# Kernel tuning notes

Hardware: AMD Instinct MI355X
Metric: run time of the kernel (lower is better)

The kernel has to match this reference:

```python
import jax, jax.numpy as jnp
import numpy as np

N_NODES = 100000
N_EDGES = 1600000
IN_C, HID_C, OUT_C = 256, 128, 256


def setup_inputs() -> dict:
    key = jax.random.key(0)
    ks = jax.random.split(key, 8)
    x = jax.random.normal(ks[0], (N_NODES, IN_C), dtype=jnp.float32)
    src = jax.random.randint(ks[1], (N_EDGES,), 0, N_NODES, dtype=jnp.int64)
    dst = jnp.sort(jax.random.randint(ks[2], (N_EDGES,), 0, N_NODES, dtype=jnp.int64))
    # GraphConv weight [in, hid] (glorot), bias [hid]
    W_conv = jax.random.normal(ks[3], (IN_C, HID_C), dtype=jnp.float32) * (2.0 / (IN_C + HID_C)) ** 0.5
    b_conv = jnp.zeros((HID_C,), dtype=jnp.float32)
    # torch Linear weights are [out, in]
    W1 = jax.random.normal(ks[4], (HID_C, HID_C), dtype=jnp.float32) * (2.0 / (2 * HID_C)) ** 0.5
    b1 = jax.random.uniform(ks[5], (HID_C,), dtype=jnp.float32, minval=-1.0, maxval=1.0) / np.sqrt(HID_C)
    W2 = jax.random.normal(ks[6], (OUT_C, HID_C), dtype=jnp.float32) * (2.0 / (HID_C + OUT_C)) ** 0.5
    b2 = jax.random.uniform(ks[7], (OUT_C,), dtype=jnp.float32, minval=-1.0, maxval=1.0) / np.sqrt(OUT_C)
    return {"x": x, "src": src, "dst": dst, "W_conv": W_conv, "b_conv": b_conv,
            "W1": W1, "b1": b1, "W2": W2, "b2": b2}


def reference(x, src, dst, W_conv, b_conv, W1, b1, W2, b2):
    N = x.shape[0]
    ones = jnp.ones(src.shape[0], dtype=x.dtype)
    out_deg = jnp.clip(jax.ops.segment_sum(ones, src, num_segments=N), 1.0)  # [N]
    in_deg = jnp.clip(jax.ops.segment_sum(ones, dst, num_segments=N), 1.0)   # [N]
    # DGL GraphConv, norm='both', in_feats > out_feats -> weight applied before aggregation
    h = x * jax.lax.rsqrt(out_deg)[:, None]          # src-side normalization
    h = h @ W_conv                                    # [N, hid]
    m = jax.ops.segment_sum(h[src], dst, num_segments=N, indices_are_sorted=True)
    h = m * jax.lax.rsqrt(in_deg)[:, None] + b_conv   # dst-side normalization + bias
    h = jax.nn.relu(h)
    h = jax.nn.relu(h @ W1.T + b1)
    return h @ W2.T + b2
```

## Files before the change

### kernel.cpp

```cpp
#include <hip/hip_runtime.h>
#include <hip/hip_bf16.h>


typedef __attribute__((ext_vector_type(8))) short short8;
typedef __attribute__((ext_vector_type(4))) float f32x4;

static __device__ __forceinline__ float bf2f(unsigned int u16) {
    union { unsigned int i; float f; } c; c.i = u16 << 16; return c.f;
}
static __device__ __forceinline__ ushort f2bf(float f) {
    union { float f; unsigned int i; } c; c.f = f;
    unsigned int i = c.i;
    return (ushort)((i + 0x7FFFu + ((i >> 16) & 1u)) >> 16);
}

constexpr int NCHUNK   = 256;
constexpr int NBUK_MAX = 512;
constexpr int WPREP_BLOCKS = (128 * 256 + 128 * 128 + 256 * 128) / 256;

__global__ __launch_bounds__(256) void prep_kernel(
    const float* __restrict__ Wc, const float* __restrict__ W1,
    const float* __restrict__ W2, ushort* __restrict__ WcT,
    ushort* __restrict__ W1b, ushort* __restrict__ W2b,
    const int* __restrict__ src, int* __restrict__ M,
    const int* __restrict__ dst, int* __restrict__ row_ptr,
    int nE, int N, int nBuk, int chunkSz)
{
    __shared__ int cnt[NBUK_MAX];
    const int bid = blockIdx.x, tid = threadIdx.x;

    if (bid < WPREP_BLOCKS) {
        int i = bid * 256 + tid;
        if (i < 128 * 256) {
            int o = i >> 8, k = i & 255;
            WcT[o * 256 + k] = f2bf(Wc[k * 128 + o]);
        } else if (i < 128 * 256 + 128 * 128) {
            int j = i - 128 * 256;
            W1b[j] = f2bf(W1[j]);
        } else {
            int j = i - 128 * 256 - 128 * 128;
            W2b[j] = f2bf(W2[j]);
        }
        return;
    }
    if (bid < WPREP_BLOCKS + NCHUNK) {
        int c = bid - WPREP_BLOCKS;
        for (int i = tid; i < nBuk; i += 256) cnt[i] = 0;
        __syncthreads();
        int e0 = c * chunkSz, e1 = min(e0 + chunkSz, nE);
        for (int e = e0 + tid; e < e1; e += 256)
            atomicAdd(&cnt[src[e] >> 8], 1);
        __syncthreads();
        for (int b = tid; b < nBuk; b += 256)
            M[b * NCHUNK + c] = cnt[b];
        return;
    }
    int e = (bid - WPREP_BLOCKS - NCHUNK) * 256 + tid;
    if (e >= nE) return;
    int d = dst[e];
    if (e == 0) {
        for (int n = 0; n <= d; ++n) row_ptr[n] = 0;
    } else {
        int p = dst[e - 1];
        for (int n = p + 1; n <= d; ++n) row_ptr[n] = e;
    }
    if (e == nE - 1) {
        for (int n = d + 1; n <= N; ++n) row_ptr[n] = nE;
    }
}

__global__ __launch_bounds__(256) void scanA_kernel(
    int* __restrict__ M, int* __restrict__ tot)
{
    __shared__ int buf[2][NCHUNK];
    int b = blockIdx.x, tid = threadIdx.x;
    int v = M[b * NCHUNK + tid];
    buf[0][tid] = v;
    __syncthreads();
    int pi = 0;
#pragma unroll
    for (int off = 1; off < NCHUNK; off <<= 1) {
        int t = buf[pi][tid];
        if (tid >= off) t += buf[pi][tid - off];
        buf[pi ^ 1][tid] = t;
        __syncthreads();
        pi ^= 1;
    }
    int incl = buf[pi][tid];
    M[b * NCHUNK + tid] = incl - v;
    if (tid == NCHUNK - 1) tot[b] = incl;
}

static __device__ __forceinline__ void scan_bb(
    const int* __restrict__ tot, int* bb_l, int nBuk, int tid)
{
    if (tid < 64) {
        int base = 0;
        for (int i0 = 0; i0 < nBuk; i0 += 64) {
            int i = i0 + tid;
            int v = (i < nBuk) ? tot[i] : 0;
            int orig = v;
#pragma unroll
            for (int off = 1; off < 64; off <<= 1) {
                int u = __shfl_up(v, off, 64);
                if (tid >= off) v += u;
            }
            if (i < nBuk) bb_l[i] = base + v - orig;
            base += __shfl(v, 63, 64);
        }
        if (tid == 0) bb_l[nBuk] = base;
    }
    __syncthreads();
}

__global__ __launch_bounds__(256) void scatter_keys_kernel(
    const int* __restrict__ src, const int* __restrict__ M,
    const int* __restrict__ tot, int* __restrict__ ss,
    int nE, int nBuk, int chunkSz)
{
    __shared__ int cur[NBUK_MAX];
    __shared__ int bb_l[NBUK_MAX + 1];
    int c = blockIdx.x, tid = threadIdx.x;
    scan_bb(tot, bb_l, nBuk, tid);
    for (int i = tid; i < nBuk; i += 256)
        cur[i] = M[i * NCHUNK + c] + bb_l[i];
    __syncthreads();
    int e0 = c * chunkSz, e1 = min(e0 + chunkSz, nE);
    for (int e = e0 + tid; e < e1; e += 256) {
        int s = src[e];
        int pos = atomicAdd(&cur[s >> 8], 1);
        ss[pos] = s;
    }
}

__global__ __launch_bounds__(512, 4) void gemm1_kernel(
    const float* __restrict__ A, const ushort* __restrict__ B,
    const int* __restrict__ ss, const int* __restrict__ tot,
    ushort* __restrict__ C, int nRows, int nBuk)
{
    __shared__ ushort Bs[128 * 256];
    __shared__ ushort As[128 * 32];
    __shared__ int hist[128];
    __shared__ int eRange[2];

    const int tid  = threadIdx.x;
    const int lane = tid & 63;
    const int w    = tid >> 6;
    const int wm   = w >> 1;
    const int wn   = w & 1;
    const int r    = lane & 15;
    const int q    = lane >> 4;
    const int row0 = blockIdx.x * 128;

#pragma unroll
    for (int s = 0; s < 8; ++s) {
        int idx = s * 512 + tid;
        int col = idx >> 5, kg = idx & 31;
        *(short8*)&Bs[col * 256 + ((kg ^ (col & 7)) * 8)] =
            *(const short8*)&B[(size_t)col * 256 + kg * 8];
    }
    if (tid < 128) hist[tid] = 0;

    if (w == 0) {
        int bk = blockIdx.x >> 1;
        int partial = 0;
        for (int i = lane; i < bk; i += 64) partial += tot[i];
#pragma unroll
        for (int off = 32; off >= 1; off >>= 1)
            partial += __shfl_xor(partial, off, 64);
        if (lane == 0) {
            eRange[0] = partial;
            eRange[1] = partial + tot[bk];
        }
    }

    const int arow = tid >> 2, akg = tid & 3;
    const int aslot = (akg ^ ((arow >> 1) & 3)) * 8;

    float4 areg[3][2];

#define G1_ISSUE(cc, bb)                                                     \
    {                                                                        \
        int g0 = row0 + arow;                                                \
        areg[bb][0] = make_float4(0.f, 0.f, 0.f, 0.f);                       \
        areg[bb][1] = make_float4(0.f, 0.f, 0.f, 0.f);                       \
        if (g0 < nRows) {                                                    \
            const float* p = &A[(size_t)g0 * 256 + (cc) * 32 + akg * 8];     \
            areg[bb][0] = *(const float4*)p;                                 \
            areg[bb][1] = *(const float4*)(p + 4);                           \
        }                                                                    \
    }

    G1_ISSUE(0, 0)
    G1_ISSUE(1, 1)
    G1_ISSUE(2, 2)
    __syncthreads();

    {
        int e0 = eRange[0], e1 = eRange[1];
        for (int e = e0 + tid; e < e1; e += 512) {
            int s = ss[e];
            if ((s >> 7) == blockIdx.x)
                atomicAdd(&hist[s & 127], 1);
        }
    }

    f32x4 acc[8];
#pragma unroll
    for (int t = 0; t < 8; ++t) acc[t] = (f32x4){0.f, 0.f, 0.f, 0.f};

#pragma unroll
    for (int c = 0; c < 8; ++c) {
        if (c > 0) __syncthreads();
        const int buf = c % 3;
        {
            float4 v0 = areg[buf][0], v1 = areg[buf][1];
            ushort u[8];
            u[0] = f2bf(v0.x); u[1] = f2bf(v0.y); u[2] = f2bf(v0.z); u[3] = f2bf(v0.w);
            u[4] = f2bf(v1.x); u[5] = f2bf(v1.y); u[6] = f2bf(v1.z); u[7] = f2bf(v1.w);
            *(short8*)&As[arow * 32 + aslot] = *(const short8*)u;
        }
        if (c + 3 < 8) G1_ISSUE(c + 3, buf)
        __syncthreads();
        {
            int ra0 = wm * 32 + r, ra1 = wm * 32 + 16 + r;
            short8 a0 = *(const short8*)&As[ra0 * 32 + ((q ^ ((ra0 >> 1) & 3)) * 8)];
            short8 a1 = *(const short8*)&As[ra1 * 32 + ((q ^ ((ra1 >> 1) & 3)) * 8)];
            int sB = c * 4 + q;
#pragma unroll
            for (int t = 0; t < 4; ++t) {
                int col = wn * 64 + t * 16 + r;
                short8 b = *(const short8*)&Bs[col * 256 + ((sB ^ (col & 7)) * 8)];
                acc[t]     = __builtin_amdgcn_mfma_f32_16x16x32_bf16(a0, b, acc[t], 0, 0, 0);
                acc[4 + t] = __builtin_amdgcn_mfma_f32_16x16x32_bf16(a1, b, acc[4 + t], 0, 0, 0);
            }
        }
    }
#undef G1_ISSUE

#pragma unroll
    for (int fr = 0; fr < 2; ++fr)
#pragma unroll
        for (int t = 0; t < 4; ++t) {
            int col = wn * 64 + t * 16 + r;
#pragma unroll
            for (int reg = 0; reg < 4; ++reg) {
                int lr = wm * 32 + fr * 16 + q * 4 + reg;
                int g = row0 + lr;
                if (g < nRows) {
                    float sc = rsqrtf((float)max(hist[lr], 1));
                    C[(size_t)g * 128 + col] = f2bf(acc[fr * 4 + t][reg] * sc);
                }
            }
        }
}

static __device__ __forceinline__ void acc8(float* a, uint4 u) {
    union { unsigned int i; float f; } c;
    c.i = u.x << 16;          a[0] += c.f;
    c.i = u.x & 0xffff0000u;  a[1] += c.f;
    c.i = u.y << 16;          a[2] += c.f;
    c.i = u.y & 0xffff0000u;  a[3] += c.f;
    c.i = u.z << 16;          a[4] += c.f;
    c.i = u.z & 0xffff0000u;  a[5] += c.f;
    c.i = u.w << 16;          a[6] += c.f;
    c.i = u.w & 0xffff0000u;  a[7] += c.f;
}

__global__ __launch_bounds__(256) void gather_kernel(
    const ushort* __restrict__ h1, const int* __restrict__ src,
    const int* __restrict__ rp, const float* __restrict__ b_conv,
    ushort* __restrict__ h2, int N)
{
    int n = (blockIdx.x * 256 + threadIdx.x) >> 6;
    int lane = threadIdx.x & 63;
    if (n >= N) return;
    const int g = lane >> 4;
    const int c = lane & 15;
    int e0 = rp[n], e1 = rp[n + 1];

    float a[8];
#pragma unroll
    for (int j = 0; j < 8; ++j) a[j] = 0.f;

    int e = e0 + g;
    for (; e + 12 < e1; e += 16) {
        int s0 = src[e], s1 = src[e + 4], s2 = src[e + 8], s3 = src[e + 12];
        uint4 u0 = *(const uint4*)&h1[((size_t)(unsigned)s0 << 7) + c * 8];
        uint4 u1 = *(const uint4*)&h1[((size_t)(unsigned)s1 << 7) + c * 8];
        uint4 u2 = *(const uint4*)&h1[((size_t)(unsigned)s2 << 7) + c * 8];
        uint4 u3 = *(const uint4*)&h1[((size_t)(unsigned)s3 << 7) + c * 8];
        acc8(a, u0); acc8(a, u1); acc8(a, u2); acc8(a, u3);
    }
    for (; e < e1; e += 4) {
        uint4 u0 = *(const uint4*)&h1[((size_t)(unsigned)src[e] << 7) + c * 8];
        acc8(a, u0);
    }

#pragma unroll
    for (int j = 0; j < 8; ++j) {
        a[j] += __shfl_xor(a[j], 16, 64);
        a[j] += __shfl_xor(a[j], 32, 64);
    }

    if (g == 0) {
        float sc = rsqrtf((float)max(e1 - e0, 1));
        ushort o[8];
#pragma unroll
        for (int j = 0; j < 8; ++j)
            o[j] = f2bf(fmaxf(fmaf(a[j], sc, b_conv[c * 8 + j]), 0.f));
        *(short8*)&h2[((size_t)(unsigned)n << 7) + c * 8] = *(const short8*)o;
    }
}

__global__ __launch_bounds__(512) void gemm23_kernel(
    const ushort* __restrict__ A, const ushort* __restrict__ W1b,
    const ushort* __restrict__ W2b, const float* __restrict__ b1,
    const float* __restrict__ b2, float* __restrict__ out, int nRows)
{
    __shared__ ushort AsTs[128 * 128];
    __shared__ ushort Ws[128 * 128];

    const int tid  = threadIdx.x;
    const int lane = tid & 63;
    const int w    = tid >> 6;
    const int wm   = w >> 1;
    const int wn   = w & 1;
    const int r    = lane & 15;
    const int q    = lane >> 4;
    const int row0 = blockIdx.x * 128;

#pragma unroll
    for (int s = 0; s < 4; ++s) {
        int idx = s * 512 + tid;
        int row = idx >> 4, kg = idx & 15;
        int g = row0 + row;
        short8 v = (short8){0, 0, 0, 0, 0, 0, 0, 0};
        if (g < nRows) v = *(const short8*)&A[(size_t)g * 128 + kg * 8];
        *(short8*)&AsTs[row * 128 + ((kg ^ (row & 7)) * 8)] = v;
    }
#pragma unroll
    for (int s = 0; s < 4; ++s) {
        int idx = s * 512 + tid;
        int col = idx >> 4, kg = idx & 15;
        *(short8*)&Ws[col * 128 + ((kg ^ (col & 7)) * 8)] =
            *(const short8*)&W1b[(size_t)col * 128 + kg * 8];
    }
    __syncthreads();

    f32x4 acc1[8];
#pragma unroll
    for (int t = 0; t < 8; ++t) acc1[t] = (f32x4){0.f, 0.f, 0.f, 0.f};
#pragma unroll
    for (int ks = 0; ks < 4; ++ks) {
        int sA = ks * 4 + q;
        int ra0 = wm * 32 + r, ra1 = wm * 32 + 16 + r;
        short8 a0 = *(const short8*)&AsTs[ra0 * 128 + ((sA ^ (ra0 & 7)) * 8)];
        short8 a1 = *(const short8*)&AsTs[ra1 * 128 + ((sA ^ (ra1 & 7)) * 8)];
#pragma unroll
        for (int t = 0; t < 4; ++t) {
            int col = wn * 64 + t * 16 + r;
            short8 b = *(const short8*)&Ws[col * 128 + ((sA ^ (col & 7)) * 8)];
            acc1[t]     = __builtin_amdgcn_mfma_f32_16x16x32_bf16(a0, b, acc1[t], 0, 0, 0);
            acc1[4 + t] = __builtin_amdgcn_mfma_f32_16x16x32_bf16(a1, b, acc1[4 + t], 0, 0, 0);
        }
    }
    __syncthreads();

#pragma unroll
    for (int fr = 0; fr < 2; ++fr)
#pragma unroll
        for (int t = 0; t < 4; ++t) {
            int col = wn * 64 + t * 16 + r;
            float bo = b1[col];
#pragma unroll
            for (int reg = 0; reg < 4; ++reg) {
                int row = wm * 32 + fr * 16 + q * 4 + reg;
                float v = fmaxf(acc1[fr * 4 + t][reg] + bo, 0.f);
                AsTs[row * 128 + (((col >> 3) ^ (row & 7)) * 8) + (col & 7)] = f2bf(v);
            }
        }
#pragma unroll
    for (int s = 0; s < 4; ++s) {
        int idx = s * 512 + tid;
        int col = idx >> 4, kg = idx & 15;
        *(short8*)&Ws[col * 128 + ((kg ^ (col & 7)) * 8)] =
            *(const short8*)&W2b[(size_t)col * 128 + kg * 8];
    }
    __syncthreads();

    f32x4 acc2[16];
#pragma unroll
    for (int t = 0; t < 16; ++t) acc2[t] = (f32x4){0.f, 0.f, 0.f, 0.f};
#pragma unroll
    for (int ks = 0; ks < 4; ++ks) {
        int sA = ks * 4 + q;
        int ra0 = wm * 32 + r, ra1 = wm * 32 + 16 + r;
        short8 a0 = *(const short8*)&AsTs[ra0 * 128 + ((sA ^ (ra0 & 7)) * 8)];
        short8 a1 = *(const short8*)&AsTs[ra1 * 128 + ((sA ^ (ra1 & 7)) * 8)];
#pragma unroll
        for (int t = 0; t < 4; ++t) {
            int col = wn * 64 + t * 16 + r;
            short8 b = *(const short8*)&Ws[col * 128 + ((sA ^ (col & 7)) * 8)];
            acc2[t]     = __builtin_amdgcn_mfma_f32_16x16x32_bf16(a0, b, acc2[t], 0, 0, 0);
            acc2[4 + t] = __builtin_amdgcn_mfma_f32_16x16x32_bf16(a1, b, acc2[4 + t], 0, 0, 0);
        }
    }
    __syncthreads();

#pragma unroll
    for (int s = 0; s < 4; ++s) {
        int idx = s * 512 + tid;
        int col = idx >> 4, kg = idx & 15;
        *(short8*)&Ws[col * 128 + ((kg ^ (col & 7)) * 8)] =
            *(const short8*)&W2b[(size_t)(128 + col) * 128 + kg * 8];
    }
    __syncthreads();

#pragma unroll
    for (int ks = 0; ks < 4; ++ks) {
        int sA = ks * 4 + q;
        int ra0 = wm * 32 + r, ra1 = wm * 32 + 16 + r;
        short8 a0 = *(const short8*)&AsTs[ra0 * 128 + ((sA ^ (ra0 & 7)) * 8)];
        short8 a1 = *(const short8*)&AsTs[ra1 * 128 + ((sA ^ (ra1 & 7)) * 8)];
#pragma unroll
        for (int t = 0; t < 4; ++t) {
            int col = wn * 64 + t * 16 + r;
            short8 b = *(const short8*)&Ws[col * 128 + ((sA ^ (col & 7)) * 8)];
            acc2[8 + t]  = __builtin_amdgcn_mfma_f32_16x16x32_bf16(a0, b, acc2[8 + t], 0, 0, 0);
            acc2[12 + t] = __builtin_amdgcn_mfma_f32_16x16x32_bf16(a1, b, acc2[12 + t], 0, 0, 0);
        }
    }

#pragma unroll
    for (int h = 0; h < 2; ++h)
#pragma unroll
        for (int fr = 0; fr < 2; ++fr)
#pragma unroll
            for (int t = 0; t < 4; ++t) {
                int col = h * 128 + wn * 64 + t * 16 + r;
                float bo = b2[col];
#pragma unroll
                for (int reg = 0; reg < 4; ++reg) {
                    int g = row0 + wm * 32 + fr * 16 + q * 4 + reg;
                    if (g < nRows)
                        out[(size_t)g * 256 + col] = acc2[h * 8 + fr * 4 + t][reg] + bo;
                }
            }
}

extern "C" void kernel_launch(void* const* d_in, const int* in_sizes, int n_in,
                              void* d_out, int out_size, void* d_ws, size_t ws_size,
                              hipStream_t stream)
{
    const float* x      = (const float*)d_in[0];
    const int*   src    = (const int*)d_in[1];
    const int*   dst    = (const int*)d_in[2];
    const float* W_conv = (const float*)d_in[3];
    const float* b_conv = (const float*)d_in[4];
    const float* W1     = (const float*)d_in[5];
    const float* b1     = (const float*)d_in[6];
    const float* W2     = (const float*)d_in[7];
    const float* b2     = (const float*)d_in[8];
    float* out = (float*)d_out;

    const int N  = in_sizes[0] / 256;
    const int nE = in_sizes[1];

    const int nBuk    = (N + 255) >> 8;
    const int chunkSz = (nE + NCHUNK - 1) / NCHUNK;

    ushort* h1  = (ushort*)d_ws;
    ushort* h2  = h1 + (size_t)N * 128;
    ushort* WcT = h2 + (size_t)N * 128;
    ushort* W1b = WcT + 128 * 256;
    ushort* W2b = W1b + 128 * 128;
    int* rp     = (int*)(W2b + 256 * 128);
    int* tot    = rp + (N + 1);
    int* M      = tot + nBuk;
    int* ss     = M + nBuk * NCHUNK;

    const int rowptrBlocks = (nE + 255) / 256;
    prep_kernel<<<WPREP_BLOCKS + NCHUNK + rowptrBlocks, 256, 0, stream>>>(
        W_conv, W1, W2, WcT, W1b, W2b, src, M, dst, rp, nE, N, nBuk, chunkSz);

    scanA_kernel<<<nBuk, 256, 0, stream>>>(M, tot);
    scatter_keys_kernel<<<NCHUNK, 256, 0, stream>>>(src, M, tot, ss, nE, nBuk, chunkSz);

    const int nBlocks128 = (N + 127) / 128;
    gemm1_kernel<<<nBlocks128, 512, 0, stream>>>(x, WcT, ss, tot, h1, N, nBuk);

    gather_kernel<<<(N * 64 + 255) / 256, 256, 0, stream>>>(
        h1, src, rp, b_conv, h2, N);

    gemm23_kernel<<<nBlocks128, 512, 0, stream>>>(h2, W1b, W2b, b1, b2, out, N);
}
```

Measured before the change: 164.0 us.

## Slice h1 into column-sliced layout so each XCD gathers from an L2-resident slice

gemm1 now writes its output as 8 column slices of 16 features each, laid out contiguously per slice. The gather kernel is reorganized so each block handles one slice for 4 nodes, and block id mod 8 selects the slice. Lanes now spread across edges, each reading 8 bytes, and the partial sums are reduced with shuffles. The aim is for each slice (~3.2MB) to stay cache-resident on the XCD that processes it, cutting HBM traffic from random row gathers. The costs are smaller per-request gathers, 8x redundant reads of the edge indices and row pointers, and more shuffles.

```diff
diff --git a/kernel.cpp b/kernel.cpp
--- a/kernel.cpp
+++ b/kernel.cpp
@@ -242,74 +242,75 @@
     for (int fr = 0; fr < 2; ++fr)
 #pragma unroll
         for (int t = 0; t < 4; ++t) {
-            int col = wn * 64 + t * 16 + r;
+            ushort* Cs = C + (size_t)(wn * 4 + t) * nRows * 16;
 #pragma unroll
             for (int reg = 0; reg < 4; ++reg) {
                 int lr = wm * 32 + fr * 16 + q * 4 + reg;
                 int g = row0 + lr;
                 if (g < nRows) {
                     float sc = rsqrtf((float)max(hist[lr], 1));
-                    C[(size_t)g * 128 + col] = f2bf(acc[fr * 4 + t][reg] * sc);
+                    Cs[(size_t)g * 16 + r] = f2bf(acc[fr * 4 + t][reg] * sc);
                 }
             }
         }
 }
 
-static __device__ __forceinline__ void acc8(float* a, uint4 u) {
-    union { unsigned int i; float f; } c;
-    c.i = u.x << 16;          a[0] += c.f;
-    c.i = u.x & 0xffff0000u;  a[1] += c.f;
-    c.i = u.y << 16;          a[2] += c.f;
-    c.i = u.y & 0xffff0000u;  a[3] += c.f;
-    c.i = u.z << 16;          a[4] += c.f;
-    c.i = u.z & 0xffff0000u;  a[5] += c.f;
-    c.i = u.w << 16;          a[6] += c.f;
-    c.i = u.w & 0xffff0000u;  a[7] += c.f;
-}
-
 __global__ __launch_bounds__(256) void gather_kernel(
-    const ushort* __restrict__ h1, const int* __restrict__ src,
+    const ushort* __restrict__ h1s, const int* __restrict__ src,
     const int* __restrict__ rp, const float* __restrict__ b_conv,
     ushort* __restrict__ h2, int N)
 {
-    int n = (blockIdx.x * 256 + threadIdx.x) >> 6;
-    int lane = threadIdx.x & 63;
+    const int slice = blockIdx.x & 7;
+    const int n = (blockIdx.x >> 3) * 4 + (threadIdx.x >> 6);
+    const int lane = threadIdx.x & 63;
     if (n >= N) return;
-    const int g = lane >> 4;
-    const int c = lane & 15;
+    const int ei = lane >> 2;
+    const int c4 = lane & 3;
     int e0 = rp[n], e1 = rp[n + 1];
-
-    float a[8];
-#pragma unroll
-    for (int j = 0; j < 8; ++j) a[j] = 0.f;
-
-    int e = e0 + g;
-    for (; e + 12 < e1; e += 16) {
-        int s0 = src[e], s1 = src[e + 4], s2 = src[e + 8], s3 = src[e + 12];
-        uint4 u0 = *(const uint4*)&h1[((size_t)(unsigned)s0 << 7) + c * 8];
-        uint4 u1 = *(const uint4*)&h1[((size_t)(unsigned)s1 << 7) + c * 8];
-        uint4 u2 = *(const uint4*)&h1[((size_t)(unsigned)s2 << 7) + c * 8];
-        uint4 u3 = *(const uint4*)&h1[((size_t)(unsigned)s3 << 7) + c * 8];
-        acc8(a, u0); acc8(a, u1); acc8(a, u2); acc8(a, u3);
-    }
-    for (; e < e1; e += 4) {
-        uint4 u0 = *(const uint4*)&h1[((size_t)(unsigned)src[e] << 7) + c * 8];
-        acc8(a, u0);
-    }
-
-#pragma unroll
-    for (int j = 0; j < 8; ++j) {
-        a[j] += __shfl_xor(a[j], 16, 64);
-        a[j] += __shfl_xor(a[j], 32, 64);
-    }
-
-    if (g == 0) {
+    const ushort* base = h1s + (size_t)slice * N * 16 + c4 * 4;
+
+    float a0 = 0.f, a1 = 0.f, a2 = 0.f, a3 = 0.f;
+    union { unsigned int i; float f; } c;
+    int e = e0 + ei;
+    for (; e + 16 < e1; e += 32) {
+        int s0 = src[e], s1 = src[e + 16];
+        uint2 u0 = *(const uint2*)&base[(size_t)(unsigned)s0 * 16];
+        uint2 u1 = *(const uint2*)&base[(size_t)(unsigned)s1 * 16];
+        c.i = u0.x << 16;          a0 += c.f;
+        c.i = u0.x & 0xffff0000u;  a1 += c.f;
+        c.i = u0.y << 16;          a2 += c.f;
+        c.i = u0.y & 0xffff0000u;  a3 += c.f;
+        c.i = u1.x << 16;          a0 += c.f;
+        c.i = u1.x & 0xffff0000u;  a1 += c.f;
+        c.i = u1.y << 16;          a2 += c.f;
+        c.i = u1.y & 0xffff0000u;  a3 += c.f;
+    }
+    if (e < e1) {
+        uint2 u0 = *(const uint2*)&base[(size_t)(unsigned)src[e] * 16];
+        c.i = u0.x << 16;          a0 += c.f;
+        c.i = u0.x & 0xffff0000u;  a1 += c.f;
+        c.i = u0.y << 16;          a2 += c.f;
+        c.i = u0.y & 0xffff0000u;  a3 += c.f;
+    }
+
+#pragma unroll
+    for (int off = 4; off < 64; off <<= 1) {
+        a0 += __shfl_xor(a0, off, 64);
+        a1 += __shfl_xor(a1, off, 64);
+        a2 += __shfl_xor(a2, off, 64);
+        a3 += __shfl_xor(a3, off, 64);
+    }
+
+    if (ei == 0) {
         float sc = rsqrtf((float)max(e1 - e0, 1));
-        ushort o[8];
-#pragma unroll
-        for (int j = 0; j < 8; ++j)
-            o[j] = f2bf(fmaxf(fmaf(a[j], sc, b_conv[c * 8 + j]), 0.f));
-        *(short8*)&h2[((size_t)(unsigned)n << 7) + c * 8] = *(const short8*)o;
+        float4 bc = *(const float4*)&b_conv[slice * 16 + c4 * 4];
+        ushort o[4];
+        o[0] = f2bf(fmaxf(fmaf(a0, sc, bc.x), 0.f));
+        o[1] = f2bf(fmaxf(fmaf(a1, sc, bc.y), 0.f));
+        o[2] = f2bf(fmaxf(fmaf(a2, sc, bc.z), 0.f));
+        o[3] = f2bf(fmaxf(fmaf(a3, sc, bc.w), 0.f));
+        *(uint2*)&h2[(size_t)(unsigned)n * 128 + slice * 16 + c4 * 4] =
+            *(const uint2*)o;
     }
 }
 
@@ -490,7 +491,7 @@
     const int nBlocks128 = (N + 127) / 128;
     gemm1_kernel<<<nBlocks128, 512, 0, stream>>>(x, WcT, ss, tot, h1, N, nBuk);
 
-    gather_kernel<<<(N * 64 + 255) / 256, 256, 0, stream>>>(
+    gather_kernel<<<((N + 3) / 4) * 8, 256, 0, stream>>>(
         h1, src, rp, b_conv, h2, N);
 
     gemm23_kernel<<<nBlocks128, 512, 0, stream>>>(h2, W1b, W2b, b1, b2, out, N);
```

Result: slower. 319.0 us (+94.6%).
